# Kernel tuning notes

Hardware: AMD Instinct MI355X
Metric: run time of the kernel (lower is better)

## Reference

```python
import jax, jax.numpy as jnp
import numpy as np

UP = 2                # upsample_factor
FILTER_SIZE = 31      # sinc filter kernel size (odd)
CUTOFF = 0.5 / UP     # cutoff frequency (fraction of Nyquist)
LEAKY_SLOPE = 0.01    # torch F.leaky_relu default


def make_sinc_filter(cutoff_freq, filter_size):
    # matches torch: t = linspace(-filter_size//2, filter_size//2, filter_size)
    lo = (-filter_size) // 2  # Python floor division: -31//2 = -16
    hi = filter_size // 2     # 15
    t = jnp.linspace(float(lo), float(hi), filter_size)
    x, y = jnp.meshgrid(t, t, indexing='ij')
    r = jnp.sqrt(x ** 2 + y ** 2) + 1e-10
    f = jnp.sin(2.0 * np.pi * cutoff_freq * r) / (np.pi * r)
    return f / jnp.sum(f)


def _ac_coords(out_n, in_n, dtype):
    # align_corners=True mapping: src = i * (in_n - 1) / (out_n - 1)
    scale = (in_n - 1) / (out_n - 1)
    c = jnp.arange(out_n, dtype=dtype) * jnp.asarray(scale, dtype)
    i0 = jnp.clip(jnp.floor(c).astype(jnp.int32), 0, in_n - 2)
    w = c - i0.astype(dtype)
    return i0, w


def bilinear_ac(x, out_h, out_w):
    # x: [B, C, H, W] -> [B, C, out_h, out_w], bilinear, align_corners=True
    H, W = x.shape[-2], x.shape[-1]
    i0, wy = _ac_coords(out_h, H, x.dtype)
    j0, wx = _ac_coords(out_w, W, x.dtype)
    # rows
    top = x[:, :, i0, :]
    bot = x[:, :, i0 + 1, :]
    xr = top + (bot - top) * wy[:, None]          # [B, C, out_h, W]
    # cols
    left = xr[:, :, :, j0]
    right = xr[:, :, :, j0 + 1]
    return left + (right - left) * wx             # [B, C, out_h, out_w]


def setup_inputs() -> dict:
    key = jax.random.key(0)
    x = jax.random.normal(key, (8, 64, 128, 128), dtype=jnp.float32)
    filt = make_sinc_filter(CUTOFF, FILTER_SIZE).astype(jnp.float32)  # buffer, deterministic
    return {"x": x, "filt": filt}


def reference(x, filt):
    B, C, H, W = x.shape
    k = filt.shape[0]
    up = bilinear_ac(x, H * UP, W * UP)
    # 2) elementwise activation
    act = jax.nn.leaky_relu(up, LEAKY_SLOPE)
    # 3) depthwise sinc low-pass conv, same padding
    kernel = jnp.broadcast_to(filt[None, None], (C, 1, k, k))  # [C,1,k,k]
    filtered = jax.lax.conv_general_dilated(
        act, kernel,
        window_strides=(1, 1),
        padding=[(k // 2, k // 2), (k // 2, k // 2)],
        feature_group_count=C,
        dimension_numbers=('NCHW', 'OIHW', 'NCHW'),
    )
    # 4) bilinear downsample back to original size (align_corners=True)
    return bilinear_ac(filtered, H, W)
```

## Files before the change

### kernel.cpp

```cpp
#include <hip/hip_runtime.h>
#include <hip/hip_bf16.h>

typedef __attribute__((ext_vector_type(8))) short bf16x8;
typedef __attribute__((ext_vector_type(16))) float f32x16;

#define INH   128
#define LEAK  0.01f
#define GSTR  288
#define TSTR  200
#define TROWS 158

__device__ __forceinline__ unsigned short f2bf(float f) {
    __hip_bfloat16 h = __float2bfloat16(f);
    return *(unsigned short*)&h;
}

__device__ __forceinline__ float upsample_one(const float* __restrict__ xc,
                                              int ur, int uc, float UPS) {
    float cr = (float)ur * UPS;
    int r0 = (int)cr; if (r0 > 126) r0 = 126;
    float wr = cr - (float)r0;
    float cs = (float)uc * UPS;
    int s0 = (int)cs; if (s0 > 126) s0 = 126;
    float ws = cs - (float)s0;
    const float* p = xc + r0 * INH + s0;
    float a = p[0], b = p[1], c = p[INH], d = p[INH + 1];
    float top = a + (c - a) * wr;
    float bot = b + (d - b) * wr;
    float val = top + (bot - top) * ws;
    return (val > 0.0f) ? val : (LEAK * val);
}

__global__ void build_table(const float* __restrict__ filt, unsigned short* __restrict__ tab) {
    int idx = blockIdx.x * 256 + threadIdx.x;
    if (idx >= 31 * 4 * 64) return;
    int lane = idx & 63, c = (idx >> 6) & 3, fr = idx >> 8;
    #pragma unroll
    for (int t = 0; t < 8; ++t) {
        int v = 16 * c + 8 * (lane >> 5) + t - (lane & 31);
        float f = (v >= 0 && v <= 30) ? filt[fr * 31 + v] : 0.0f;
        tab[idx * 8 + t] = f2bf(f);
    }
}

__global__ __launch_bounds__(256)
void up_table(const float* __restrict__ x, const float* __restrict__ filt,
              unsigned short* __restrict__ U, unsigned short* __restrict__ tab) {
    const int tid = threadIdx.x;
    if (blockIdx.x < 31) {
        int idx = blockIdx.x * 256 + tid;
        if (idx >= 31 * 4 * 64) return;
        int lane = idx & 63, c = (idx >> 6) & 3, fr = idx >> 8;
        #pragma unroll
        for (int t = 0; t < 8; ++t) {
            int v = 16 * c + 8 * (lane >> 5) + t - (lane & 31);
            float f = (v >= 0 && v <= 30) ? filt[fr * 31 + v] : 0.0f;
            tab[idx * 8 + t] = f2bf(f);
        }
        return;
    }
    const float UPS = (float)(127.0 / 255.0);
    int idx = (blockIdx.x - 31) * 256 + tid;
    int bc = idx / (256 * 72);
    int rem = idx - bc * (256 * 72);
    int r = rem / 72;
    int c4 = (rem - r * 72) * 4;
    const float* __restrict__ xc = x + (size_t)bc * (INH * INH);
    unsigned short o[4];
    #pragma unroll
    for (int e = 0; e < 4; ++e) {
        int uc = c4 + e - 15;
        float val = 0.0f;
        if ((unsigned)uc < 256u) val = upsample_one(xc, r, uc, UPS);
        o[e] = f2bf(val);
    }
    *(uint2*)&U[((size_t)bc * 256 + r) * GSTR + c4] = *(const uint2*)o;
}

__global__ __launch_bounds__(256, 2)
void conv_ds(const unsigned short* __restrict__ U, const unsigned short* __restrict__ tab,
             float* __restrict__ out) {
    __shared__ unsigned short T[TROWS * TSTR];
    const int tid = threadIdx.x;
    const int bx = blockIdx.x;
    const int by = blockIdx.y;
    const int bc = blockIdx.z;
    const float DNS = (float)(255.0 / 127.0);
    const unsigned short* __restrict__ Ub = U + (size_t)bc * 256 * GSTR + bx * 128;

    #pragma unroll
    for (int k = 0; k < 13; ++k) {
        int c = tid + k * 256;
        if (c < TROWS * 20) {
            int row = c / 20;
            int sub = c - row * 20;
            int gr = 128 * by + row - 15;
            uint4 v = {0u, 0u, 0u, 0u};
            if ((unsigned)gr < 256u)
                v = *(const uint4*)(Ub + gr * GSTR + sub * 8);
            *(uint4*)&T[row * TSTR + sub * 8] = v;
        }
    }
    __syncthreads();

    const int lane = tid & 63;
    const int w = tid >> 6;
    const int r32 = lane & 31;
    const int hk = lane >> 5;

    const char* ab = (const char*)T + (32 * w + r32) * (TSTR * 2) + hk * 16;
    const bf16x8* tv = (const bf16x8*)tab;

    f32x16 acc[4];
    #pragma unroll
    for (int s = 0; s < 4; ++s)
        acc[s] = (f32x16){0.f,0.f,0.f,0.f,0.f,0.f,0.f,0.f,0.f,0.f,0.f,0.f,0.f,0.f,0.f,0.f};

    #pragma unroll 1
    for (int fr = 0; fr < 31; ++fr) {
        bf16x8 B[4];
        #pragma unroll
        for (int km = 0; km < 4; ++km)
            B[km] = tv[(fr * 4 + km) * 64 + lane];
        const char* u = ab + fr * (TSTR * 2);
        bf16x8 A[10];
        #pragma unroll
        for (int c = 0; c < 10; ++c)
            A[c] = *(const bf16x8*)(u + c * 32);
        #pragma unroll
        for (int km = 0; km < 4; ++km)
            #pragma unroll
            for (int s = 0; s < 4; ++s)
                acc[s] = __builtin_amdgcn_mfma_f32_32x32x16_bf16(A[2 * s + km], B[km], acc[s], 0, 0, 0);
    }

    #pragma unroll
    for (int s = 0; s < 4; ++s) {
        int cc = 128 * bx + 32 * s + r32;
        const bool doout = (cc & 1) == 0;
        const int oj = cc >> 1;
        const float wxw = (float)oj * DNS - (float)cc;
        #pragma unroll
        for (int p = 0; p < 8; ++p) {
            int rpe = ((p & 1) << 1) + ((p >> 1) << 3) + 4 * hk;
            int cre = 128 * by + 32 * w + rpe;
            int oi = cre >> 1;
            float wyw = (float)oi * DNS - (float)cre;
            float ae = acc[s][2 * p], ao = acc[s][2 * p + 1];
            float v = ae + (ao - ae) * wyw;
            float vr = __shfl_xor(v, 1, 64);
            if (doout) {
                float o = v + (vr - v) * wxw;
                out[((size_t)bc * 128 + oi) * 128 + oj] = o;
            }
        }
    }
}

#define FUSTR  120
#define FUROWS 158
__global__ __launch_bounds__(256)
void afa_mfma(const float* __restrict__ x, const unsigned short* __restrict__ tab,
              float* __restrict__ out) {
    __shared__ unsigned short Ut[FUROWS * FUSTR];
    const int tid = threadIdx.x;
    const int bx = blockIdx.x, by = blockIdx.y, bc = blockIdx.z;
    const float* __restrict__ xc = x + (size_t)bc * (INH * INH);
    const float UPS = (float)(127.0 / 255.0);
    const float DNS = (float)(255.0 / 127.0);
    const int pr0 = 128 * by, pc0 = 64 * bx;

    for (int idx = tid; idx < FUROWS * (FUSTR / 2); idx += 256) {
        int lr = idx / (FUSTR / 2);
        int lc0 = (idx - lr * (FUSTR / 2)) * 2;
        unsigned pack = 0;
        #pragma unroll
        for (int e = 0; e < 2; ++e) {
            int lc = lc0 + e;
            int ur = pr0 + lr - 15;
            int uc = pc0 + lc - 15;
            float val = 0.0f;
            if (lc < 96 && (unsigned)ur < 256u && (unsigned)uc < 256u)
                val = upsample_one(xc, ur, uc, UPS);
            pack |= (unsigned)f2bf(val) << (16 * e);
        }
        *(unsigned*)&Ut[lr * FUSTR + lc0] = pack;
    }
    __syncthreads();

    const int lane = tid & 63;
    const int w = tid >> 6;
    const int wxs = w & 1, wys = w >> 1;
    const int r32 = lane & 31;
    const int hk = lane >> 5;
    const char* ub = (const char*)Ut + (64 * wys + r32) * (FUSTR * 2) + (32 * wxs + 8 * hk) * 2;
    const bf16x8* tv = (const bf16x8*)tab;
    f32x16 acc0 = {0.f,0.f,0.f,0.f,0.f,0.f,0.f,0.f,0.f,0.f,0.f,0.f,0.f,0.f,0.f,0.f};
    f32x16 acc1 = acc0;

    #pragma unroll 1
    for (int fr = 0; fr < 31; ++fr) {
        bf16x8 B0 = tv[(fr * 4 + 0) * 64 + lane];
        bf16x8 B1 = tv[(fr * 4 + 1) * 64 + lane];
        bf16x8 B2 = tv[(fr * 4 + 2) * 64 + lane];
        bf16x8 B3 = tv[(fr * 4 + 3) * 64 + lane];
        const char* u0 = ub + fr * (FUSTR * 2);
        const char* u1 = u0 + 32 * (FUSTR * 2);
        bf16x8 a;
        a = *(const bf16x8*)(u0 + 0);
        acc0 = __builtin_amdgcn_mfma_f32_32x32x16_bf16(a, B0, acc0, 0, 0, 0);
        a = *(const bf16x8*)(u0 + 32);
        acc0 = __builtin_amdgcn_mfma_f32_32x32x16_bf16(a, B1, acc0, 0, 0, 0);
        a = *(const bf16x8*)(u0 + 64);
        acc0 = __builtin_amdgcn_mfma_f32_32x32x16_bf16(a, B2, acc0, 0, 0, 0);
        a = *(const bf16x8*)(u0 + 96);
        acc0 = __builtin_amdgcn_mfma_f32_32x32x16_bf16(a, B3, acc0, 0, 0, 0);
        a = *(const bf16x8*)(u1 + 0);
        acc1 = __builtin_amdgcn_mfma_f32_32x32x16_bf16(a, B0, acc1, 0, 0, 0);
        a = *(const bf16x8*)(u1 + 32);
        acc1 = __builtin_amdgcn_mfma_f32_32x32x16_bf16(a, B1, acc1, 0, 0, 0);
        a = *(const bf16x8*)(u1 + 64);
        acc1 = __builtin_amdgcn_mfma_f32_32x32x16_bf16(a, B2, acc1, 0, 0, 0);
        a = *(const bf16x8*)(u1 + 96);
        acc1 = __builtin_amdgcn_mfma_f32_32x32x16_bf16(a, B3, acc1, 0, 0, 0);
    }

    const int cc = 64 * bx + 32 * wxs + r32;
    const bool doout = (cc & 1) == 0;
    const int oj = cc >> 1;
    const float wxw = (float)oj * DNS - (float)cc;
    #pragma unroll
    for (int tt = 0; tt < 2; ++tt) {
        int cr0 = 128 * by + 64 * wys + 32 * tt;
        #pragma unroll
        for (int p = 0; p < 8; ++p) {
            int rpe = ((p & 1) << 1) + ((p >> 1) << 3) + 4 * hk;
            int cre = cr0 + rpe;
            int oi = cre >> 1;
            float wyw = (float)oi * DNS - (float)cre;
            float ae, ao;
            if (tt == 0) { ae = acc0[2 * p]; ao = acc0[2 * p + 1]; }
            else         { ae = acc1[2 * p]; ao = acc1[2 * p + 1]; }
            float v = ae + (ao - ae) * wyw;
            float vr = __shfl_xor(v, 1, 64);
            if (doout) {
                float o = v + (vr - v) * wxw;
                out[((size_t)bc * 128 + oi) * 128 + oj] = o;
            }
        }
    }
}

extern "C" void kernel_launch(void* const* d_in, const int* in_sizes, int n_in,
                              void* d_out, int out_size, void* d_ws, size_t ws_size,
                              hipStream_t stream) {
    const float* x    = (const float*)d_in[0];
    const float* filt = (const float*)d_in[1];
    float* out = (float*)d_out;

    unsigned short* tab = (unsigned short*)d_ws;
    const size_t U_OFF  = 131072;
    const size_t U_NEED = U_OFF + (size_t)512 * 256 * GSTR * 2;

    if (ws_size >= U_NEED) {
        unsigned short* U = (unsigned short*)((char*)d_ws + U_OFF);
        up_table<<<31 + 512 * 256 * 72 / 256, 256, 0, stream>>>(x, filt, U, tab);
        dim3 grid(2, 2, 8 * 64);
        conv_ds<<<grid, dim3(256), 0, stream>>>(U, tab, out);
    } else {
        build_table<<<31, 256, 0, stream>>>(filt, tab);
        dim3 grid(4, 2, 8 * 64);
        afa_mfma<<<grid, dim3(256), 0, stream>>>(x, tab, out);
    }
}
```

Measured before the change: 171.9 us.

## Retile conv MFMA into 2x2 wave blocks with double-buffered inline-asm loads

New measurement: 165.5 us. 1.04x faster.

```diff
diff --git a/kernel.cpp b/kernel.cpp
--- a/kernel.cpp
+++ b/kernel.cpp
@@ -7,7 +7,7 @@
 #define INH   128
 #define LEAK  0.01f
 #define GSTR  288
-#define TSTR  200
+#define TSTR  168
 #define TROWS 158
 
 __device__ __forceinline__ unsigned short f2bf(float f) {
@@ -77,6 +77,39 @@
     *(uint2*)&U[((size_t)bc * 256 + r) * GSTR + c4] = *(const uint2*)o;
 }
 
+#define DSRD(dst, addr, OFF) \
+    asm volatile("ds_read_b128 %0, %1 offset:" #OFF : "=v"(dst) : "v"(addr))
+#define GLB(dst, p, OFF) \
+    asm volatile("global_load_dwordx4 %0, %1, off offset:" #OFF : "=v"(dst) : "v"(p))
+
+#define ISSUE(u, p, A00,A01,A02,A03,A04,A05, A10,A11,A12,A13,A14,A15, B0,B1,B2,B3) { \
+    DSRD(A00,u,0);     DSRD(A01,u,32);    DSRD(A02,u,64); \
+    DSRD(A03,u,96);    DSRD(A04,u,128);   DSRD(A05,u,160); \
+    DSRD(A10,u,10752); DSRD(A11,u,10784); DSRD(A12,u,10816); \
+    DSRD(A13,u,10848); DSRD(A14,u,10880); DSRD(A15,u,10912); \
+    GLB(B0,p,0); GLB(B1,p,1024); GLB(B2,p,2048); GLB(B3,p,3072); }
+
+#define WAIT_SET { asm volatile("s_waitcnt vmcnt(4) lgkmcnt(12)"); __builtin_amdgcn_sched_barrier(0); }
+#define WAIT_END { asm volatile("s_waitcnt vmcnt(0) lgkmcnt(0)");  __builtin_amdgcn_sched_barrier(0); }
+
+#define MFMA16(A00,A01,A02,A03,A04,A05, A10,A11,A12,A13,A14,A15, B0,B1,B2,B3) { \
+    acc00 = __builtin_amdgcn_mfma_f32_32x32x16_bf16(A00, B0, acc00, 0, 0, 0); \
+    acc10 = __builtin_amdgcn_mfma_f32_32x32x16_bf16(A10, B0, acc10, 0, 0, 0); \
+    acc01 = __builtin_amdgcn_mfma_f32_32x32x16_bf16(A02, B0, acc01, 0, 0, 0); \
+    acc11 = __builtin_amdgcn_mfma_f32_32x32x16_bf16(A12, B0, acc11, 0, 0, 0); \
+    acc00 = __builtin_amdgcn_mfma_f32_32x32x16_bf16(A01, B1, acc00, 0, 0, 0); \
+    acc10 = __builtin_amdgcn_mfma_f32_32x32x16_bf16(A11, B1, acc10, 0, 0, 0); \
+    acc01 = __builtin_amdgcn_mfma_f32_32x32x16_bf16(A03, B1, acc01, 0, 0, 0); \
+    acc11 = __builtin_amdgcn_mfma_f32_32x32x16_bf16(A13, B1, acc11, 0, 0, 0); \
+    acc00 = __builtin_amdgcn_mfma_f32_32x32x16_bf16(A02, B2, acc00, 0, 0, 0); \
+    acc10 = __builtin_amdgcn_mfma_f32_32x32x16_bf16(A12, B2, acc10, 0, 0, 0); \
+    acc01 = __builtin_amdgcn_mfma_f32_32x32x16_bf16(A04, B2, acc01, 0, 0, 0); \
+    acc11 = __builtin_amdgcn_mfma_f32_32x32x16_bf16(A14, B2, acc11, 0, 0, 0); \
+    acc00 = __builtin_amdgcn_mfma_f32_32x32x16_bf16(A03, B3, acc00, 0, 0, 0); \
+    acc10 = __builtin_amdgcn_mfma_f32_32x32x16_bf16(A13, B3, acc10, 0, 0, 0); \
+    acc01 = __builtin_amdgcn_mfma_f32_32x32x16_bf16(A05, B3, acc01, 0, 0, 0); \
+    acc11 = __builtin_amdgcn_mfma_f32_32x32x16_bf16(A15, B3, acc11, 0, 0, 0); }
+
 __global__ __launch_bounds__(256, 2)
 void conv_ds(const unsigned short* __restrict__ U, const unsigned short* __restrict__ tab,
              float* __restrict__ out) {
@@ -105,53 +138,64 @@
 
     const int lane = tid & 63;
     const int w = tid >> 6;
+    const int wx = w & 1;
+    const int wr = w >> 1;
     const int r32 = lane & 31;
     const int hk = lane >> 5;
 
-    const char* ab = (const char*)T + (32 * w + r32) * (TSTR * 2) + hk * 16;
-    const bf16x8* tv = (const bf16x8*)tab;
-
-    f32x16 acc[4];
-    #pragma unroll
-    for (int s = 0; s < 4; ++s)
-        acc[s] = (f32x16){0.f,0.f,0.f,0.f,0.f,0.f,0.f,0.f,0.f,0.f,0.f,0.f,0.f,0.f,0.f,0.f};
+    const char* ab = (const char*)T + (64 * wr + r32) * (TSTR * 2) + (128 * wx + 16 * hk);
+    const unsigned ux = (unsigned)(unsigned long long)(const void*)ab;
+    const char* pb0 = (const char*)tab + (size_t)lane * 16;
+
+    f32x16 acc00 = {0.f,0.f,0.f,0.f,0.f,0.f,0.f,0.f,0.f,0.f,0.f,0.f,0.f,0.f,0.f,0.f};
+    f32x16 acc01 = acc00, acc10 = acc00, acc11 = acc00;
+
+    bf16x8 xA00,xA01,xA02,xA03,xA04,xA05, xA10,xA11,xA12,xA13,xA14,xA15, xB0,xB1,xB2,xB3;
+    bf16x8 yA00,yA01,yA02,yA03,yA04,yA05, yA10,yA11,yA12,yA13,yA14,yA15, yB0,yB1,yB2,yB3;
+
+    ISSUE(ux, pb0, xA00,xA01,xA02,xA03,xA04,xA05, xA10,xA11,xA12,xA13,xA14,xA15, xB0,xB1,xB2,xB3);
 
     #pragma unroll 1
-    for (int fr = 0; fr < 31; ++fr) {
-        bf16x8 B[4];
+    for (int it = 0; it < 15; ++it) {
+        unsigned uy = ux + (unsigned)(2 * it + 1) * 336;
+        const char* py = pb0 + (size_t)(2 * it + 1) * 4096;
+        ISSUE(uy, py, yA00,yA01,yA02,yA03,yA04,yA05, yA10,yA11,yA12,yA13,yA14,yA15, yB0,yB1,yB2,yB3);
+        WAIT_SET;
+        MFMA16(xA00,xA01,xA02,xA03,xA04,xA05, xA10,xA11,xA12,xA13,xA14,xA15, xB0,xB1,xB2,xB3);
+        unsigned ux2 = ux + (unsigned)(2 * it + 2) * 336;
+        const char* px = pb0 + (size_t)(2 * it + 2) * 4096;
+        ISSUE(ux2, px, xA00,xA01,xA02,xA03,xA04,xA05, xA10,xA11,xA12,xA13,xA14,xA15, xB0,xB1,xB2,xB3);
+        WAIT_SET;
+        MFMA16(yA00,yA01,yA02,yA03,yA04,yA05, yA10,yA11,yA12,yA13,yA14,yA15, yB0,yB1,yB2,yB3);
+    }
+    WAIT_END;
+    MFMA16(xA00,xA01,xA02,xA03,xA04,xA05, xA10,xA11,xA12,xA13,xA14,xA15, xB0,xB1,xB2,xB3);
+
+    #pragma unroll
+    for (int rr = 0; rr < 2; ++rr) {
         #pragma unroll
-        for (int km = 0; km < 4; ++km)
-            B[km] = tv[(fr * 4 + km) * 64 + lane];
-        const char* u = ab + fr * (TSTR * 2);
-        bf16x8 A[10];
-        #pragma unroll
-        for (int c = 0; c < 10; ++c)
-            A[c] = *(const bf16x8*)(u + c * 32);
-        #pragma unroll
-        for (int km = 0; km < 4; ++km)
+        for (int s = 0; s < 2; ++s) {
+            int cc = 128 * bx + 64 * wx + 32 * s + r32;
+            const bool doout = (cc & 1) == 0;
+            const int oj = cc >> 1;
+            const float wxw = (float)oj * DNS - (float)cc;
             #pragma unroll
-            for (int s = 0; s < 4; ++s)
-                acc[s] = __builtin_amdgcn_mfma_f32_32x32x16_bf16(A[2 * s + km], B[km], acc[s], 0, 0, 0);
-    }
-
-    #pragma unroll
-    for (int s = 0; s < 4; ++s) {
-        int cc = 128 * bx + 32 * s + r32;
-        const bool doout = (cc & 1) == 0;
-        const int oj = cc >> 1;
-        const float wxw = (float)oj * DNS - (float)cc;
-        #pragma unroll
-        for (int p = 0; p < 8; ++p) {
-            int rpe = ((p & 1) << 1) + ((p >> 1) << 3) + 4 * hk;
-            int cre = 128 * by + 32 * w + rpe;
-            int oi = cre >> 1;
-            float wyw = (float)oi * DNS - (float)cre;
-            float ae = acc[s][2 * p], ao = acc[s][2 * p + 1];
-            float v = ae + (ao - ae) * wyw;
-            float vr = __shfl_xor(v, 1, 64);
-            if (doout) {
-                float o = v + (vr - v) * wxw;
-                out[((size_t)bc * 128 + oi) * 128 + oj] = o;
+            for (int p = 0; p < 8; ++p) {
+                int rpe = ((p & 1) << 1) + ((p >> 1) << 3) + 4 * hk;
+                int cre = 128 * by + 64 * wr + 32 * rr + rpe;
+                int oi = cre >> 1;
+                float wyw = (float)oi * DNS - (float)cre;
+                float ae, ao;
+                if (rr == 0 && s == 0)      { ae = acc00[2 * p]; ao = acc00[2 * p + 1]; }
+                else if (rr == 0 && s == 1) { ae = acc01[2 * p]; ao = acc01[2 * p + 1]; }
+                else if (rr == 1 && s == 0) { ae = acc10[2 * p]; ao = acc10[2 * p + 1]; }
+                else                        { ae = acc11[2 * p]; ao = acc11[2 * p + 1]; }
+                float v = ae + (ao - ae) * wyw;
+                float vr = __shfl_xor(v, 1, 64);
+                if (doout) {
+                    float o = v + (vr - v) * wxw;
+                    out[((size_t)bc * 128 + oi) * 128 + oj] = o;
+                }
             }
         }
     }
```
